# Performance work log

Hardware: AMD Instinct MI355X
Metric: run time of the kernel (lower is better)

The kernel has to match this reference:

```python
import jax, jax.numpy as jnp
import numpy as np

D = 1024
LD = 64
NTR = 8192
NT = 8192
DY = 128

def setup_inputs() -> dict:
    key = jax.random.key(0)
    k1, k2, k3, k4 = jax.random.split(key, 4)
    xtr = jax.random.normal(k1, (NTR, D), dtype=jnp.float32)
    ytr = jax.random.normal(k2, (NTR, DY), dtype=jnp.float32)
    xt = jax.random.normal(k3, (NT, D), dtype=jnp.float32)
    A = jax.random.normal(k4, (D, LD), dtype=jnp.float32) / (D ** 0.5)
    return {"xtr": xtr, "ytr": ytr, "xt": xt, "A": A}

def reference(xtr, ytr, xt, A):
    # mean-center both train and test features with the train mean
    mu = jnp.mean(xtr, axis=0, keepdims=True)          # [1, d]
    qtr = (xtr - mu) @ A                                # [Ntr, ld]
    qt = (xt - mu) @ A                                  # [Nt, ld]
    scores = jnp.einsum('nl,ml->nm', qt, qtr)           # [Nt, Ntr]
    E = jax.nn.softmax(scores, axis=1)                  # row-wise softmax over train points
    return E @ ytr                                      # [Nt, dy]
```

## Files before the change

kernel.cpp:

```cpp
#include <hip/hip_runtime.h>
#include <hip/hip_bf16.h>

#define D    1024
#define LD   64
#define NTR  8192
#define NT   8192
#define DY   128

#define SHIFT 40.0f

typedef __attribute__((ext_vector_type(8))) short bf16x8;
typedef __attribute__((ext_vector_type(8))) _Float16 half8;
typedef __attribute__((ext_vector_type(4))) short short4_;
typedef __attribute__((ext_vector_type(4))) float f4;

static __device__ __forceinline__ short f2bf(float f) {
    __hip_bfloat16 h = __float2bfloat16(f);
    short s; __builtin_memcpy(&s, &h, 2); return s;
}
static __device__ __forceinline__ float bf2f(short s) {
    __hip_bfloat16 h; __builtin_memcpy(&h, &s, 2); return __bfloat162float(h);
}
static __device__ __forceinline__ short f2h(float f) {
    _Float16 h = (_Float16)f;
    short s; __builtin_memcpy(&s, &h, 2); return s;
}
static __device__ __forceinline__ float h2f(short s) {
    _Float16 h; __builtin_memcpy(&h, &s, 2); return (float)h;
}

static __device__ __forceinline__ void gload_lds16(const void* g, void* l) {
    __builtin_amdgcn_global_load_lds(
        (const __attribute__((address_space(1))) unsigned int*)g,
        (__attribute__((address_space(3))) unsigned int*)l,
        16, 0, 0);
}

__global__ __launch_bounds__(256) void a_prep(const float* __restrict__ A,
                                              short* __restrict__ Afh,
                                              short* __restrict__ Afl) {
    int idx = blockIdx.x * 256 + threadIdx.x;
    float a = A[idx];
    int k = idx >> 6;
    int col = idx & 63;
    short hi = f2bf(a);
    short lo = f2bf(a - bf2f(hi));
    int o = ((k >> 6) * 8 + ((k >> 5) & 1) * 4 + ((k >> 3) & 3)) * 512
          + col * 8 + (k & 7);
    Afh[o] = hi;
    Afl[o] = lo;
}

__global__ __launch_bounds__(256) void proj_prep(const float* __restrict__ xt,
                                                 const float* __restrict__ xtr,
                                                 const short* __restrict__ Afh,
                                                 const short* __restrict__ Afl,
                                                 const float* __restrict__ ytr,
                                                 short* __restrict__ qt_hi,
                                                 short* __restrict__ qt_lo,
                                                 short* __restrict__ ktr,
                                                 float* __restrict__ muAp,
                                                 short* __restrict__ vtile) {
    __shared__ __align__(16) char smraw[17408];

    int tid = threadIdx.x;
    int b = blockIdx.x;

    if (b >= 1024) {
        float* tile = (float*)smraw;
        int bz = b - 1024;
        int t0 = (bz & 127) * 64;
        int d0 = (bz >> 7) * 64;
        int c = tid & 63;
        int r4 = tid >> 6;
        #pragma unroll
        for (int i = 0; i < 16; ++i) {
            int r = i * 4 + r4;
            tile[r * 66 + c] = ytr[(long)(t0 + r) * DY + d0 + c];
        }
        __syncthreads();
        #pragma unroll
        for (int i = 0; i < 16; ++i) {
            int r = i * 4 + r4;
            int t = t0 + c;
            int dy = d0 + r;
            long idx = (long)(t >> 5) * 4096 + (long)dy * 32
                     + ((((t >> 3) & 3) ^ (dy & 3)) << 3) + (t & 7);
            vtile[idx] = f2bf(tile[c * 66 + r]);
        }
        return;
    }

    short (*xh)[16][136] = (short (*)[16][136])smraw;
    short (*xl)[16][136] = (short (*)[16][136])(smraw + 8704);

    int wave = tid >> 6;
    int lane = tid & 63;
    int quad = lane >> 4;
    int l16 = lane & 15;

    bool is_test = b < (NT / 16);
    int row0 = (is_test ? b : b - NT / 16) * 16;
    const float* x = is_test ? xt : xtr;

    int crow = tid >> 4;
    int cgrp = tid & 15;
    const float* xg = x + (long)(row0 + crow) * D + cgrp * 8;

    int col = wave * 16 + l16;
    const short* AfhL = Afh + quad * 512 + col * 8;
    const short* AflL = Afl + quad * 512 + col * 8;

    f4 acc = (f4){0.f, 0.f, 0.f, 0.f};

    {
        f4 v0 = *(const f4*)xg;
        f4 v1 = *(const f4*)(xg + 4);
        short4_ h0, h1, lo0, lo1;
        #pragma unroll
        for (int e = 0; e < 4; ++e) {
            h0[e] = f2bf(v0[e]);  lo0[e] = f2bf(v0[e] - bf2f(h0[e]));
            h1[e] = f2bf(v1[e]);  lo1[e] = f2bf(v1[e] - bf2f(h1[e]));
        }
        *(short4_*)&xh[0][crow][cgrp * 8]     = h0;
        *(short4_*)&xh[0][crow][cgrp * 8 + 4] = h1;
        *(short4_*)&xl[0][crow][cgrp * 8]     = lo0;
        *(short4_*)&xl[0][crow][cgrp * 8 + 4] = lo1;
    }
    __syncthreads();

    #pragma unroll 1
    for (int s = 0; s < 8; ++s) {
        int cur = s & 1;

        f4 nv0, nv1;
        if (s < 7) {
            nv0 = *(const f4*)(xg + (s + 1) * 128);
            nv1 = *(const f4*)(xg + (s + 1) * 128 + 4);
        }

        const short* xhr = &xh[cur][l16][0];
        const short* xlr = &xl[cur][l16][0];

        #pragma unroll
        for (int s2 = 0; s2 < 2; ++s2) {
            int s2g = s * 2 + s2;

            bf16x8 bh0 = *(const bf16x8*)(AfhL + s2g * 4096);
            bf16x8 bh1 = *(const bf16x8*)(AfhL + s2g * 4096 + 2048);
            bf16x8 bl0 = *(const bf16x8*)(AflL + s2g * 4096);
            bf16x8 bl1 = *(const bf16x8*)(AflL + s2g * 4096 + 2048);

            bf16x8 ah0 = *(const bf16x8*)(xhr + s2 * 64 + quad * 8);
            bf16x8 ah1 = *(const bf16x8*)(xhr + s2 * 64 + 32 + quad * 8);
            bf16x8 al0 = *(const bf16x8*)(xlr + s2 * 64 + quad * 8);
            bf16x8 al1 = *(const bf16x8*)(xlr + s2 * 64 + 32 + quad * 8);

            acc = __builtin_amdgcn_mfma_f32_16x16x32_bf16(ah0, bh0, acc, 0, 0, 0);
            acc = __builtin_amdgcn_mfma_f32_16x16x32_bf16(al0, bh0, acc, 0, 0, 0);
            acc = __builtin_amdgcn_mfma_f32_16x16x32_bf16(ah0, bl0, acc, 0, 0, 0);
            acc = __builtin_amdgcn_mfma_f32_16x16x32_bf16(ah1, bh1, acc, 0, 0, 0);
            acc = __builtin_amdgcn_mfma_f32_16x16x32_bf16(al1, bh1, acc, 0, 0, 0);
            acc = __builtin_amdgcn_mfma_f32_16x16x32_bf16(ah1, bl1, acc, 0, 0, 0);
        }

        if (s < 7) {
            short4_ h0, h1, lo0, lo1;
            #pragma unroll
            for (int e = 0; e < 4; ++e) {
                h0[e] = f2bf(nv0[e]);  lo0[e] = f2bf(nv0[e] - bf2f(h0[e]));
                h1[e] = f2bf(nv1[e]);  lo1[e] = f2bf(nv1[e] - bf2f(h1[e]));
            }
            *(short4_*)&xh[cur ^ 1][crow][cgrp * 8]     = h0;
            *(short4_*)&xh[cur ^ 1][crow][cgrp * 8 + 4] = h1;
            *(short4_*)&xl[cur ^ 1][crow][cgrp * 8]     = lo0;
            *(short4_*)&xl[cur ^ 1][crow][cgrp * 8 + 4] = lo1;
        }
        __syncthreads();
    }

    #pragma unroll
    for (int r = 0; r < 4; ++r) {
        int grow = row0 + quad * 4 + r;
        float qv = acc[r];
        if (is_test) {
            short hi = f2h(qv);
            qt_hi[(long)grow * LD + col] = hi;
            qt_lo[(long)grow * LD + col] = f2h(qv - h2f(hi));
        } else {
            int tl = grow & 31;
            long idx = (long)(grow >> 5) * 2048 + tl * 64
                     + ((((col >> 3) ^ (tl & 7))) << 3) + (col & 7);
            ktr[idx] = f2h(qv);
        }
    }

    if (!is_test) {
        float s = acc[0] + acc[1] + acc[2] + acc[3];
        s += __shfl_xor(s, 16);
        s += __shfl_xor(s, 32);
        if (quad == 0) muAp[(long)(b - NT / 16) * 64 + col] = s;
    }
}

__global__ __launch_bounds__(256) void c_kernel(const short* __restrict__ ktr,
                                                const float* __restrict__ muAp,
                                                float* __restrict__ cc) {
    __shared__ float red[4][64];
    __shared__ __align__(16) float muAs[64];
    int l = threadIdx.x & 63;
    int g = threadIdx.x >> 6;
    float ms = 0.f;
    #pragma unroll 8
    for (int p = g; p < 512; p += 4) ms += muAp[(long)p * 64 + l];
    red[g][l] = ms;
    __syncthreads();
    if (threadIdx.x < 64)
        muAs[l] = (red[0][l] + red[1][l] + red[2][l] + red[3][l]) *
                  (1.0f / (float)NTR);
    __syncthreads();

    int t = blockIdx.x * 256 + threadIdx.x;
    int tl = t & 31;
    long rb = (long)(t >> 5) * 2048 + tl * 64;
    float s = SHIFT;
    #pragma unroll
    for (int c = 0; c < 8; ++c) {
        int pos = (c ^ (tl & 7)) << 3;
        bf16x8 h8 = *(const bf16x8*)&ktr[rb + pos];
        f4 m0 = *(const f4*)&muAs[c * 8];
        f4 m1 = *(const f4*)&muAs[c * 8 + 4];
        #pragma unroll
        for (int j = 0; j < 4; ++j) {
            s += h2f(h8[j]) * m0[j];
            s += h2f(h8[j + 4]) * m1[j];
        }
    }
    cc[t] = s;
}

template<int NC>
__global__ __launch_bounds__(256, 3) void flash_kernel(const short* __restrict__ qt_hi,
                                                       const short* __restrict__ qt_lo,
                                                       const short* __restrict__ ksw,
                                                       const short* __restrict__ vtile,
                                                       const float* __restrict__ cc,
                                                       short* __restrict__ Opart,
                                                       float* __restrict__ Lpart) {
    constexpr int TPC = 256 / NC;
    constexpr int CH  = NTR / NC;

    __shared__ __align__(16) short kbh[2][2048];
    __shared__ __align__(16) short vbuf[2][4096];
    __shared__ __align__(16) short ptile[4][1280];

    int tid = threadIdx.x;
    int wave = tid >> 6;
    int lane = tid & 63;
    int quad = lane >> 4;
    int l16 = lane & 15;

    int kc = blockIdx.x & (NC - 1);
    int qi = blockIdx.x / NC;
    int q0w = qi * 128 + wave * 32;
    int tile0 = kc * TPC;
    int kc0 = kc * CH;

    int soff = wave * 512 + lane * 8;
    int ldso = wave * 512;

    half8 qh[2][2], ql[2][2];
    #pragma unroll
    for (int rt = 0; rt < 2; ++rt) {
        const short* qrh = qt_hi + (long)(q0w + rt * 16 + l16) * LD + quad * 8;
        const short* qrl = qt_lo + (long)(q0w + rt * 16 + l16) * LD + quad * 8;
        qh[rt][0] = *(const half8*)qrh;
        qh[rt][1] = *(const half8*)(qrh + 32);
        ql[rt][0] = *(const half8*)qrl;
        ql[rt][1] = *(const half8*)(qrl + 32);
    }

    bf16x8 onef;
    #pragma unroll
    for (int i = 0; i < 8; ++i) onef[i] = (short)0x3F80;

    f4 Ov[2][8];
    f4 Lv[2];
    #pragma unroll
    for (int rt = 0; rt < 2; ++rt) {
        Lv[rt] = (f4){0.f, 0.f, 0.f, 0.f};
        #pragma unroll
        for (int jt = 0; jt < 8; ++jt) Ov[rt][jt] = (f4){0.f, 0.f, 0.f, 0.f};
    }

    short* myp = &ptile[wave][0];
    const int p0 = ((quad ^ (l16 & 7)) << 3);
    const int pv = ((quad ^ (l16 & 3)) << 3);

    gload_lds16(ksw + (long)tile0 * 2048 + soff, &kbh[0][ldso]);
    gload_lds16(vtile + (long)tile0 * 4096 + soff, &vbuf[0][ldso]);
    gload_lds16(vtile + (long)tile0 * 4096 + 2048 + soff, &vbuf[0][2048 + ldso]);
    __syncthreads();

    #pragma unroll 1
    for (int it = 0; it < TPC; ++it) {
        int cur = it & 1;

        f4 cv[2];
        #pragma unroll
        for (int tt = 0; tt < 2; ++tt)
            cv[tt] = *(const f4*)&cc[kc0 + it * 32 + tt * 16 + quad * 4];

        if (it < TPC - 1) {
            int nb = cur ^ 1;
            long tb = (long)(tile0 + it + 1);
            gload_lds16(ksw + tb * 2048 + soff, &kbh[nb][ldso]);
            gload_lds16(vtile + tb * 4096 + soff, &vbuf[nb][ldso]);
            gload_lds16(vtile + tb * 4096 + 2048 + soff, &vbuf[nb][2048 + ldso]);
        }

        half8 kh[2][2];
        #pragma unroll
        for (int tt = 0; tt < 2; ++tt) {
            int rb = (tt * 16 + l16) * 64;
            kh[tt][0] = *(const half8*)&kbh[cur][rb + p0];
            kh[tt][1] = *(const half8*)&kbh[cur][rb + (p0 ^ 32)];
        }

        f4 s[2][2];
        #pragma unroll
        for (int rt = 0; rt < 2; ++rt) {
            #pragma unroll
            for (int tt = 0; tt < 2; ++tt) {
                f4 a = (f4){0.f, 0.f, 0.f, 0.f};
                a = __builtin_amdgcn_mfma_f32_16x16x32_f16(kh[tt][0], qh[rt][0], a, 0, 0, 0);
                a = __builtin_amdgcn_mfma_f32_16x16x32_f16(kh[tt][0], ql[rt][0], a, 0, 0, 0);
                a = __builtin_amdgcn_mfma_f32_16x16x32_f16(kh[tt][1], qh[rt][1], a, 0, 0, 0);
                a = __builtin_amdgcn_mfma_f32_16x16x32_f16(kh[tt][1], ql[rt][1], a, 0, 0, 0);
                s[rt][tt] = a;
            }
        }

        #pragma unroll
        for (int rt = 0; rt < 2; ++rt) {
            #pragma unroll
            for (int tt = 0; tt < 2; ++tt) {
                short4_ p4;
                p4[0] = f2bf(__expf(s[rt][tt][0] - cv[tt][0]));
                p4[1] = f2bf(__expf(s[rt][tt][1] - cv[tt][1]));
                p4[2] = f2bf(__expf(s[rt][tt][2] - cv[tt][2]));
                p4[3] = f2bf(__expf(s[rt][tt][3] - cv[tt][3]));
                *(short4_*)&myp[(rt * 16 + l16) * 40 + tt * 16 + quad * 4] = p4;
            }
        }

        bf16x8 vf[8];
        #pragma unroll
        for (int jt = 0; jt < 8; ++jt)
            vf[jt] = *(const bf16x8*)&vbuf[cur][(jt * 16 + l16) * 32 + pv];
        #pragma unroll
        for (int rt = 0; rt < 2; ++rt) {
            bf16x8 pf = *(const bf16x8*)&myp[(rt * 16 + l16) * 40 + quad * 8];
            #pragma unroll
            for (int jt = 0; jt < 8; ++jt)
                Ov[rt][jt] = __builtin_amdgcn_mfma_f32_16x16x32_bf16(pf, vf[jt], Ov[rt][jt], 0, 0, 0);
            Lv[rt] = __builtin_amdgcn_mfma_f32_16x16x32_bf16(pf, onef, Lv[rt], 0, 0, 0);
        }

        __syncthreads();
    }

    long ob = (long)kc * NT;
    #pragma unroll
    for (int rt = 0; rt < 2; ++rt) {
        #pragma unroll
        for (int jt = 0; jt < 8; ++jt) {
            #pragma unroll
            for (int r = 0; r < 4; ++r)
                Opart[(ob + q0w + rt * 16 + quad * 4 + r) * DY + jt * 16 + l16] =
                    f2bf(Ov[rt][jt][r]);
        }
        if (l16 == 0) {
            #pragma unroll
            for (int r = 0; r < 4; ++r)
                Lpart[ob + q0w + rt * 16 + quad * 4 + r] = Lv[rt][r];
        }
    }
}

template<int NC>
__global__ __launch_bounds__(256) void finalize_kernel(const short* __restrict__ Opart,
                                                       const float* __restrict__ Lpart,
                                                       float* __restrict__ out) {
    long i = ((long)blockIdx.x * 256 + threadIdx.x) * 8;
    long row = i >> 7;
    float L = 0.f;
    f4 a = (f4){0.f, 0.f, 0.f, 0.f};
    f4 b = (f4){0.f, 0.f, 0.f, 0.f};
    #pragma unroll
    for (int kc = 0; kc < NC; ++kc) {
        L += Lpart[(long)kc * NT + row];
        bf16x8 o = *(const bf16x8*)&Opart[(long)kc * NT * DY + i];
        #pragma unroll
        for (int j = 0; j < 4; ++j) {
            a[j] += bf2f(o[j]);
            b[j] += bf2f(o[j + 4]);
        }
    }
    float linv = 1.0f / L;
    a *= linv; b *= linv;
    *(f4*)&out[i] = a;
    *(f4*)&out[i + 4] = b;
}

extern "C" void kernel_launch(void* const* d_in, const int* in_sizes, int n_in,
                              void* d_out, int out_size, void* d_ws, size_t ws_size,
                              hipStream_t stream) {
    const float* xtr = (const float*)d_in[0];
    const float* ytr = (const float*)d_in[1];
    const float* xt  = (const float*)d_in[2];
    const float* A   = (const float*)d_in[3];
    float* out = (float*)d_out;

    const size_t need16 =
        (size_t)512 * 64 * 4 + (size_t)NTR * 4 +
        (size_t)16 * NT * 4 + (size_t)16 * NT * DY * 2 +
        (size_t)NT * LD * 2 * 2 + (size_t)NTR * LD * 2 +
        (size_t)DY * NTR * 2 + (size_t)D * LD * 2 * 2;
    const int NC = (ws_size >= need16) ? 16 : 8;

    char* w = (char*)d_ws;
    float* muAp  = (float*)w; w += (size_t)512 * 64 * 4;
    float* cc    = (float*)w; w += (size_t)NTR * 4;
    float* Lpart = (float*)w; w += (size_t)NC * NT * 4;
    short* Opart = (short*)w; w += (size_t)NC * NT * DY * 2;
    short* qt_hi  = (short*)w; w += (size_t)NT * LD * 2;
    short* qt_lo  = (short*)w; w += (size_t)NT * LD * 2;
    short* ksw    = (short*)w; w += (size_t)NTR * LD * 2;
    short* vtile  = (short*)w; w += (size_t)DY * NTR * 2;
    short* Afh    = (short*)w; w += (size_t)D * LD * 2;
    short* Afl    = (short*)w; w += (size_t)D * LD * 2;
    (void)in_sizes; (void)n_in; (void)out_size;

    a_prep<<<256, 256, 0, stream>>>(A, Afh, Afl);
    proj_prep<<<1280, 256, 0, stream>>>(xt, xtr, Afh, Afl, ytr,
                                        qt_hi, qt_lo, ksw, muAp, vtile);
    c_kernel<<<32, 256, 0, stream>>>(ksw, muAp, cc);
    if (NC == 16) {
        flash_kernel<16><<<64 * 16, 256, 0, stream>>>(qt_hi, qt_lo, ksw, vtile,
                                                      cc, Opart, Lpart);
        finalize_kernel<16><<<(NT * DY) / (256 * 8), 256, 0, stream>>>(Opart,
                                                                       Lpart, out);
    } else {
        flash_kernel<8><<<64 * 8, 256, 0, stream>>>(qt_hi, qt_lo, ksw, vtile,
                                                    cc, Opart, Lpart);
        finalize_kernel<8><<<(NT * DY) / (256 * 8), 256, 0, stream>>>(Opart,
                                                                      Lpart, out);
    }
}
```

Measured before the change: 164.9 us.

## Process 32 rows per projection block to reuse A fragments, with XOR-swizzled LDS

The projection kernel now handles 32 input rows per block instead of 16, so each A-fragment load from global memory feeds two row tiles of MFMAs. This halves the number of projection blocks and A reloads, and the c_kernel partial-sum loop is shortened to match. The LDS staging is widened to 16-byte stores, and the padded layout is replaced by an XOR swizzle to avoid bank conflicts. In exchange the kernel uses more LDS and registers per block and launches fewer blocks, which may reduce occupancy and latency hiding.

```diff
diff --git a/kernel.cpp b/kernel.cpp
--- a/kernel.cpp
+++ b/kernel.cpp
@@ -61,14 +61,14 @@
                                                  short* __restrict__ ktr,
                                                  float* __restrict__ muAp,
                                                  short* __restrict__ vtile) {
-    __shared__ __align__(16) char smraw[17408];
+    __shared__ __align__(16) char smraw[32768];
 
     int tid = threadIdx.x;
     int b = blockIdx.x;
 
-    if (b >= 1024) {
+    if (b >= 512) {
         float* tile = (float*)smraw;
-        int bz = b - 1024;
+        int bz = b - 512;
         int t0 = (bz & 127) * 64;
         int d0 = (bz >> 7) * 64;
         int c = tid & 63;
@@ -91,41 +91,52 @@
         return;
     }
 
-    short (*xh)[16][136] = (short (*)[16][136])smraw;
-    short (*xl)[16][136] = (short (*)[16][136])(smraw + 8704);
+    short (*xh)[32][128] = (short (*)[32][128])smraw;
+    short (*xl)[32][128] = (short (*)[32][128])(smraw + 16384);
 
     int wave = tid >> 6;
     int lane = tid & 63;
     int quad = lane >> 4;
     int l16 = lane & 15;
 
-    bool is_test = b < (NT / 16);
-    int row0 = (is_test ? b : b - NT / 16) * 16;
+    bool is_test = b < 256;
+    int row0 = (is_test ? b : b - 256) * 32;
     const float* x = is_test ? xt : xtr;
 
-    int crow = tid >> 4;
-    int cgrp = tid & 15;
-    const float* xg = x + (long)(row0 + crow) * D + cgrp * 8;
+    int crow = tid >> 3;
+    int cg0 = tid & 7;
+    const float* xg = x + (long)(row0 + crow) * D + cg0 * 8;
+    int sw0 = ((cg0)     ^ (crow & 7)) * 8;
+    int sw1 = ((cg0 + 8) ^ (crow & 7)) * 8;
 
     int col = wave * 16 + l16;
     const short* AfhL = Afh + quad * 512 + col * 8;
     const short* AflL = Afl + quad * 512 + col * 8;
 
-    f4 acc = (f4){0.f, 0.f, 0.f, 0.f};
+    f4 acc[2][2];
+    #pragma unroll
+    for (int rt = 0; rt < 2; ++rt)
+        #pragma unroll
+        for (int s2 = 0; s2 < 2; ++s2)
+            acc[rt][s2] = (f4){0.f, 0.f, 0.f, 0.f};
 
     {
         f4 v0 = *(const f4*)xg;
         f4 v1 = *(const f4*)(xg + 4);
-        short4_ h0, h1, lo0, lo1;
+        f4 v2 = *(const f4*)(xg + 64);
+        f4 v3 = *(const f4*)(xg + 68);
+        bf16x8 h0, l0, h1, l1;
         #pragma unroll
         for (int e = 0; e < 4; ++e) {
-            h0[e] = f2bf(v0[e]);  lo0[e] = f2bf(v0[e] - bf2f(h0[e]));
-            h1[e] = f2bf(v1[e]);  lo1[e] = f2bf(v1[e] - bf2f(h1[e]));
-        }
-        *(short4_*)&xh[0][crow][cgrp * 8]     = h0;
-        *(short4_*)&xh[0][crow][cgrp * 8 + 4] = h1;
-        *(short4_*)&xl[0][crow][cgrp * 8]     = lo0;
-        *(short4_*)&xl[0][crow][cgrp * 8 + 4] = lo1;
+            h0[e]     = f2bf(v0[e]);  l0[e]     = f2bf(v0[e] - bf2f(h0[e]));
+            h0[e + 4] = f2bf(v1[e]);  l0[e + 4] = f2bf(v1[e] - bf2f(h0[e + 4]));
+            h1[e]     = f2bf(v2[e]);  l1[e]     = f2bf(v2[e] - bf2f(h1[e]));
+            h1[e + 4] = f2bf(v3[e]);  l1[e + 4] = f2bf(v3[e] - bf2f(h1[e + 4]));
+        }
+        *(bf16x8*)&xh[0][crow][sw0] = h0;
+        *(bf16x8*)&xl[0][crow][sw0] = l0;
+        *(bf16x8*)&xh[0][crow][sw1] = h1;
+        *(bf16x8*)&xl[0][crow][sw1] = l1;
     }
     __syncthreads();
 
@@ -133,14 +144,14 @@
     for (int s = 0; s < 8; ++s) {
         int cur = s & 1;
 
-        f4 nv0, nv1;
+        f4 nv0, nv1, nv2, nv3;
         if (s < 7) {
-            nv0 = *(const f4*)(xg + (s + 1) * 128);
-            nv1 = *(const f4*)(xg + (s + 1) * 128 + 4);
-        }
-
-        const short* xhr = &xh[cur][l16][0];
-        const short* xlr = &xl[cur][l16][0];
+            const float* ng = xg + (s + 1) * 128;
+            nv0 = *(const f4*)ng;
+            nv1 = *(const f4*)(ng + 4);
+            nv2 = *(const f4*)(ng + 64);
+            nv3 = *(const f4*)(ng + 68);
+        }
 
         #pragma unroll
         for (int s2 = 0; s2 < 2; ++s2) {
@@ -151,55 +162,71 @@
             bf16x8 bl0 = *(const bf16x8*)(AflL + s2g * 4096);
             bf16x8 bl1 = *(const bf16x8*)(AflL + s2g * 4096 + 2048);
 
-            bf16x8 ah0 = *(const bf16x8*)(xhr + s2 * 64 + quad * 8);
-            bf16x8 ah1 = *(const bf16x8*)(xhr + s2 * 64 + 32 + quad * 8);
-            bf16x8 al0 = *(const bf16x8*)(xlr + s2 * 64 + quad * 8);
-            bf16x8 al1 = *(const bf16x8*)(xlr + s2 * 64 + 32 + quad * 8);
-
-            acc = __builtin_amdgcn_mfma_f32_16x16x32_bf16(ah0, bh0, acc, 0, 0, 0);
-            acc = __builtin_amdgcn_mfma_f32_16x16x32_bf16(al0, bh0, acc, 0, 0, 0);
-            acc = __builtin_amdgcn_mfma_f32_16x16x32_bf16(ah0, bl0, acc, 0, 0, 0);
-            acc = __builtin_amdgcn_mfma_f32_16x16x32_bf16(ah1, bh1, acc, 0, 0, 0);
-            acc = __builtin_amdgcn_mfma_f32_16x16x32_bf16(al1, bh1, acc, 0, 0, 0);
-            acc = __builtin_amdgcn_mfma_f32_16x16x32_bf16(ah1, bl1, acc, 0, 0, 0);
+            int ch0 = s2 * 8 + quad;
+            int sx0 = ((ch0)     ^ (l16 & 7)) * 8;
+            int sx1 = ((ch0 + 4) ^ (l16 & 7)) * 8;
+
+            #pragma unroll
+            for (int rt = 0; rt < 2; ++rt) {
+                const short* xhr = &xh[cur][rt * 16 + l16][0];
+                const short* xlr = &xl[cur][rt * 16 + l16][0];
+                bf16x8 ah0 = *(const bf16x8*)(xhr + sx0);
+                bf16x8 ah1 = *(const bf16x8*)(xhr + sx1);
+                bf16x8 al0 = *(const bf16x8*)(xlr + sx0);
+                bf16x8 al1 = *(const bf16x8*)(xlr + sx1);
+
+                acc[rt][s2] = __builtin_amdgcn_mfma_f32_16x16x32_bf16(ah0, bh0, acc[rt][s2], 0, 0, 0);
+                acc[rt][s2] = __builtin_amdgcn_mfma_f32_16x16x32_bf16(al0, bh0, acc[rt][s2], 0, 0, 0);
+                acc[rt][s2] = __builtin_amdgcn_mfma_f32_16x16x32_bf16(ah0, bl0, acc[rt][s2], 0, 0, 0);
+                acc[rt][s2] = __builtin_amdgcn_mfma_f32_16x16x32_bf16(ah1, bh1, acc[rt][s2], 0, 0, 0);
+                acc[rt][s2] = __builtin_amdgcn_mfma_f32_16x16x32_bf16(al1, bh1, acc[rt][s2], 0, 0, 0);
+                acc[rt][s2] = __builtin_amdgcn_mfma_f32_16x16x32_bf16(ah1, bl1, acc[rt][s2], 0, 0, 0);
+            }
         }
 
         if (s < 7) {
-            short4_ h0, h1, lo0, lo1;
+            bf16x8 h0, l0, h1, l1;
             #pragma unroll
             for (int e = 0; e < 4; ++e) {
-                h0[e] = f2bf(nv0[e]);  lo0[e] = f2bf(nv0[e] - bf2f(h0[e]));
-                h1[e] = f2bf(nv1[e]);  lo1[e] = f2bf(nv1[e] - bf2f(h1[e]));
+                h0[e]     = f2bf(nv0[e]);  l0[e]     = f2bf(nv0[e] - bf2f(h0[e]));
+                h0[e + 4] = f2bf(nv1[e]);  l0[e + 4] = f2bf(nv1[e] - bf2f(h0[e + 4]));
+                h1[e]     = f2bf(nv2[e]);  l1[e]     = f2bf(nv2[e] - bf2f(h1[e]));
+                h1[e + 4] = f2bf(nv3[e]);  l1[e + 4] = f2bf(nv3[e] - bf2f(h1[e + 4]));
             }
-            *(short4_*)&xh[cur ^ 1][crow][cgrp * 8]     = h0;
-            *(short4_*)&xh[cur ^ 1][crow][cgrp * 8 + 4] = h1;
-            *(short4_*)&xl[cur ^ 1][crow][cgrp * 8]     = lo0;
-            *(short4_*)&xl[cur ^ 1][crow][cgrp * 8 + 4] = lo1;
+            *(bf16x8*)&xh[cur ^ 1][crow][sw0] = h0;
+            *(bf16x8*)&xl[cur ^ 1][crow][sw0] = l0;
+            *(bf16x8*)&xh[cur ^ 1][crow][sw1] = h1;
+            *(bf16x8*)&xl[cur ^ 1][crow][sw1] = l1;
         }
         __syncthreads();
     }
 
     #pragma unroll
-    for (int r = 0; r < 4; ++r) {
-        int grow = row0 + quad * 4 + r;
-        float qv = acc[r];
-        if (is_test) {
-            short hi = f2h(qv);
-            qt_hi[(long)grow * LD + col] = hi;
-            qt_lo[(long)grow * LD + col] = f2h(qv - h2f(hi));
-        } else {
-            int tl = grow & 31;
-            long idx = (long)(grow >> 5) * 2048 + tl * 64
-                     + ((((col >> 3) ^ (tl & 7))) << 3) + (col & 7);
-            ktr[idx] = f2h(qv);
+    for (int rt = 0; rt < 2; ++rt) {
+        f4 q4 = acc[rt][0] + acc[rt][1];
+        #pragma unroll
+        for (int r = 0; r < 4; ++r) {
+            int grow = row0 + rt * 16 + quad * 4 + r;
+            float qv = q4[r];
+            if (is_test) {
+                short hi = f2h(qv);
+                qt_hi[(long)grow * LD + col] = hi;
+                qt_lo[(long)grow * LD + col] = f2h(qv - h2f(hi));
+            } else {
+                int tl = grow & 31;
+                long idx = (long)(grow >> 5) * 2048 + tl * 64
+                         + ((((col >> 3) ^ (tl & 7))) << 3) + (col & 7);
+                ktr[idx] = f2h(qv);
+            }
         }
     }
 
     if (!is_test) {
-        float s = acc[0] + acc[1] + acc[2] + acc[3];
+        f4 t4 = (acc[0][0] + acc[0][1]) + (acc[1][0] + acc[1][1]);
+        float s = t4[0] + t4[1] + t4[2] + t4[3];
         s += __shfl_xor(s, 16);
         s += __shfl_xor(s, 32);
-        if (quad == 0) muAp[(long)(b - NT / 16) * 64 + col] = s;
+        if (quad == 0) muAp[(long)(b - 256) * 64 + col] = s;
     }
 }
 
@@ -212,7 +239,7 @@
     int g = threadIdx.x >> 6;
     float ms = 0.f;
     #pragma unroll 8
-    for (int p = g; p < 512; p += 4) ms += muAp[(long)p * 64 + l];
+    for (int p = g; p < 256; p += 4) ms += muAp[(long)p * 64 + l];
     red[g][l] = ms;
     __syncthreads();
     if (threadIdx.x < 64)
@@ -443,8 +470,8 @@
     (void)in_sizes; (void)n_in; (void)out_size;
 
     a_prep<<<256, 256, 0, stream>>>(A, Afh, Afl);
-    proj_prep<<<1280, 256, 0, stream>>>(xt, xtr, Afh, Afl, ytr,
-                                        qt_hi, qt_lo, ksw, muAp, vtile);
+    proj_prep<<<768, 256, 0, stream>>>(xt, xtr, Afh, Afl, ytr,
+                                       qt_hi, qt_lo, ksw, muAp, vtile);
     c_kernel<<<32, 256, 0, stream>>>(ksw, muAp, cc);
     if (NC == 16) {
         flash_kernel<16><<<64 * 16, 256, 0, stream>>>(qt_hi, qt_lo, ksw, vtile,
```

After: 161.6 us. About the same (-2.0%).
